# Kernel optimization log

Measured on AMD Instinct MI355X. Metric: run time of the kernel, lower is better.

## Reference

```python
import jax, jax.numpy as jnp
import numpy as np

B = 1024
IN_SIZE = 8192
OUT_SIZE = 8192
CONNECTIVITY = 32
NNZ = OUT_SIZE * CONNECTIVITY  # 262144


def setup_inputs() -> dict:
    key = jax.random.key(0)
    kx, kv, ki = jax.random.split(key, 3)
    x = jax.random.normal(kx, (B, IN_SIZE), dtype=jnp.float32)
    # uniform init as in module: (rand-0.5)*2*sqrt(3/connectivity)
    scale = np.sqrt(3.0 / CONNECTIVITY)
    values = (jax.random.uniform(kv, (NNZ,), dtype=jnp.float32) - 0.5) * 2.0 * scale
    # indices_out = list(range(out_size)) * connectivity -> arange(nnz) % out_size
    idx_out = (jnp.arange(NNZ) % OUT_SIZE).astype(jnp.int32)
    # uniform distribution: randperm(nnz) % in_size ~ uniform over [0, in_size)
    idx_in = jax.random.randint(ki, (NNZ,), 0, IN_SIZE, dtype=jnp.int32)
    return {"x": x, "values": values, "idx_out": idx_out, "idx_in": idx_in,
            "out_size": OUT_SIZE}


def reference(x, values, idx_out, idx_in, out_size):
    # y[b, o] = sum over nnz k with idx_out[k]==o of values[k] * x[b, idx_in[k]]
    # (spmm(indices, values, out, in, x.T).T in the original)
    contrib = x[:, idx_in] * values[None, :]          # [B, nnz]
    y = jnp.zeros((x.shape[0], out_size), dtype=x.dtype)
    y = y.at[:, idx_out].add(contrib)                 # scatter-add over output rows
    return y
```

## Files before the change

kernel.cpp:

```cpp
#include <hip/hip_runtime.h>

#define IN_SIZE   8192
#define OUT_SIZE  8192
#define CONN      32
#define NNZ       (OUT_SIZE * CONN)
#define BATCH     1024
#define BT        4
#define OT        4096
#define NTHREADS  512
#define OPT       (OT / NTHREADS)

typedef int          int4v   __attribute__((ext_vector_type(4)));
typedef float        float4v __attribute__((ext_vector_type(4)));
typedef unsigned int uint2v  __attribute__((ext_vector_type(2)));
typedef unsigned int uint4v  __attribute__((ext_vector_type(4)));

__device__ __forceinline__ unsigned bf16rne(float f) {
  unsigned u = __builtin_bit_cast(unsigned, f);
  return (u + 0x7fffu + ((u >> 16) & 1u)) >> 16;
}

__global__ __launch_bounds__(256)
void pack_kernel(const float* __restrict__ values,
                 const int*   __restrict__ idx_in,
                 unsigned int* __restrict__ pk) {
  int k = blockIdx.x * 256 + threadIdx.x;
  if (k < NNZ) {
    unsigned u = __builtin_bit_cast(unsigned, values[k]);
    unsigned r = (u + 0xFFFu + ((u >> 13) & 1u)) >> 13;
    pk[k] = ((unsigned)idx_in[k] << 19) | (r & 0x7FFFFu);
  }
}

template<bool PACKED>
__global__ __launch_bounds__(NTHREADS, 4)
void spl_kernel(const float* __restrict__ x,
                const unsigned int* __restrict__ pk,
                const float* __restrict__ values,
                const int* __restrict__ idx_in,
                float* __restrict__ y) {
  __shared__ unsigned long long xs[IN_SIZE];

  const int s  = blockIdx.x & 15;
  const int g  = blockIdx.x >> 4;
  const int oh = s >> 3;
  const int bb = g * 8 + (s & 7);
  const int b0 = bb * BT;
  const int o0 = oh * OT + threadIdx.x * OPT;

  {
    const float4v* r0 = (const float4v*)(x + (size_t)(b0 + 0) * IN_SIZE);
    const float4v* r1 = (const float4v*)(x + (size_t)(b0 + 1) * IN_SIZE);
    const float4v* r2 = (const float4v*)(x + (size_t)(b0 + 2) * IN_SIZE);
    const float4v* r3 = (const float4v*)(x + (size_t)(b0 + 3) * IN_SIZE);
    #pragma unroll
    for (int pass = 0; pass < IN_SIZE / (NTHREADS * 4); ++pass) {
      int c4 = pass * NTHREADS + threadIdx.x;
      float4v a = r0[c4], b = r1[c4], c = r2[c4], d = r3[c4];
      #pragma unroll
      for (int q = 0; q < 4; ++q) {
        unsigned lo = bf16rne(a[q]) | (bf16rne(b[q]) << 16);
        unsigned hi = bf16rne(c[q]) | (bf16rne(d[q]) << 16);
        xs[c4 * 4 + q] = ((unsigned long long)hi << 32) | lo;
      }
    }
  }
  __syncthreads();

  float acc[OPT][BT];
  #pragma unroll
  for (int q = 0; q < OPT; ++q)
    #pragma unroll
    for (int bt = 0; bt < BT; ++bt) acc[q][bt] = 0.0f;

  const char* xsb = (const char*)xs;

  #pragma unroll 2
  for (int j = 0; j < CONN; ++j) {
    const int kb = j * OUT_SIZE + o0;
    unsigned pv[OPT];
    if constexpr (PACKED) {
      uint4v p0 = *(const uint4v*)(pk + kb);
      uint4v p1 = *(const uint4v*)(pk + kb + 4);
      pv[0]=p0.x; pv[1]=p0.y; pv[2]=p0.z; pv[3]=p0.w;
      pv[4]=p1.x; pv[5]=p1.y; pv[6]=p1.z; pv[7]=p1.w;
      #pragma unroll
      for (int q = 0; q < OPT; ++q) {
        unsigned p = pv[q];
        float v = __builtin_bit_cast(float, p << 13);
        uint2v gv = *(const uint2v*)(xsb + ((p >> 16) & 0x1FFF8u));
        float x0 = __builtin_bit_cast(float, gv.x << 16);
        float x1 = __builtin_bit_cast(float, gv.x & 0xFFFF0000u);
        float x2 = __builtin_bit_cast(float, gv.y << 16);
        float x3 = __builtin_bit_cast(float, gv.y & 0xFFFF0000u);
        acc[q][0] += v * x0;
        acc[q][1] += v * x1;
        acc[q][2] += v * x2;
        acc[q][3] += v * x3;
      }
    } else {
      int4v  i0 = *(const int4v*)(idx_in + kb);
      int4v  i1 = *(const int4v*)(idx_in + kb + 4);
      float4v v0 = *(const float4v*)(values + kb);
      float4v v1 = *(const float4v*)(values + kb + 4);
      int   iv[OPT] = {i0.x,i0.y,i0.z,i0.w,i1.x,i1.y,i1.z,i1.w};
      float vv[OPT] = {v0.x,v0.y,v0.z,v0.w,v1.x,v1.y,v1.z,v1.w};
      #pragma unroll
      for (int q = 0; q < OPT; ++q) {
        float v = vv[q];
        uint2v gv = *(const uint2v*)(xsb + ((unsigned)iv[q] << 3));
        float x0 = __builtin_bit_cast(float, gv.x << 16);
        float x1 = __builtin_bit_cast(float, gv.x & 0xFFFF0000u);
        float x2 = __builtin_bit_cast(float, gv.y << 16);
        float x3 = __builtin_bit_cast(float, gv.y & 0xFFFF0000u);
        acc[q][0] += v * x0;
        acc[q][1] += v * x1;
        acc[q][2] += v * x2;
        acc[q][3] += v * x3;
      }
    }
  }

  #pragma unroll
  for (int bt = 0; bt < BT; ++bt) {
    float* yr = y + (size_t)(b0 + bt) * OUT_SIZE + o0;
    float4v w0 = {acc[0][bt], acc[1][bt], acc[2][bt], acc[3][bt]};
    float4v w1 = {acc[4][bt], acc[5][bt], acc[6][bt], acc[7][bt]};
    __builtin_nontemporal_store(w0, (float4v*)yr);
    __builtin_nontemporal_store(w1, (float4v*)(yr + 4));
  }
}

extern "C" void kernel_launch(void* const* d_in, const int* in_sizes, int n_in,
                              void* d_out, int out_size, void* d_ws, size_t ws_size,
                              hipStream_t stream) {
  const float* x      = (const float*)d_in[0];
  const float* values = (const float*)d_in[1];
  const int*   idx_in = (const int*)d_in[3];
  float*       y      = (float*)d_out;

  const dim3 grid((BATCH / BT) * (OUT_SIZE / OT));
  const dim3 blk(NTHREADS);

  if (ws_size >= (size_t)NNZ * sizeof(unsigned int)) {
    unsigned int* pk = (unsigned int*)d_ws;
    hipLaunchKernelGGL(pack_kernel, dim3(NNZ / 256), dim3(256), 0, stream,
                       values, idx_in, pk);
    hipLaunchKernelGGL((spl_kernel<true>), grid, blk, 0, stream,
                       x, pk, values, idx_in, y);
  } else {
    hipLaunchKernelGGL((spl_kernel<false>), grid, blk, 0, stream,
                       x, nullptr, values, idx_in, y);
  }
}
```

Baseline: 36.19 us.

## Tile eight batch rows per block with 128-bit LDS gathers and permuted index layout

Doubles the batch tile to eight rows packed as bf16 into 16-byte LDS entries (128 KB shared per block) and doubles the thread count, so each output row handles four outputs instead of eight. Each LDS gather now feeds eight FMAs instead of four, halving gather instructions and the number of passes over the index/value stream. The LDS layout is permuted (index split by low two bits) so the staging writes are contiguous, and the pack kernel pre-permutes indices to match. The trade-off is one block per CU due to LDS size, lower occupancy, and a serialised staging phase without the grid swizzle used before.

```diff
diff --git a/kernel.cpp b/kernel.cpp
--- a/kernel.cpp
+++ b/kernel.cpp
@@ -5,14 +5,13 @@
 #define CONN      32
 #define NNZ       (OUT_SIZE * CONN)
 #define BATCH     1024
-#define BT        4
+#define BT        8
 #define OT        4096
-#define NTHREADS  512
+#define NTHREADS  1024
 #define OPT       (OT / NTHREADS)
 
 typedef int          int4v   __attribute__((ext_vector_type(4)));
 typedef float        float4v __attribute__((ext_vector_type(4)));
-typedef unsigned int uint2v  __attribute__((ext_vector_type(2)));
 typedef unsigned int uint4v  __attribute__((ext_vector_type(4)));
 
 __device__ __forceinline__ unsigned bf16rne(float f) {
@@ -28,41 +27,43 @@
   if (k < NNZ) {
     unsigned u = __builtin_bit_cast(unsigned, values[k]);
     unsigned r = (u + 0xFFFu + ((u >> 13) & 1u)) >> 13;
-    pk[k] = ((unsigned)idx_in[k] << 19) | (r & 0x7FFFFu);
+    unsigned i = (unsigned)idx_in[k];
+    unsigned s = ((i & 3u) << 11) | (i >> 2);
+    pk[k] = (s << 19) | (r & 0x7FFFFu);
   }
 }
 
 template<bool PACKED>
-__global__ __launch_bounds__(NTHREADS, 4)
+__global__ __launch_bounds__(NTHREADS)
 void spl_kernel(const float* __restrict__ x,
                 const unsigned int* __restrict__ pk,
                 const float* __restrict__ values,
                 const int* __restrict__ idx_in,
                 float* __restrict__ y) {
-  __shared__ unsigned long long xs[IN_SIZE];
+  __shared__ uint4v xs[IN_SIZE];
 
-  const int s  = blockIdx.x & 15;
-  const int g  = blockIdx.x >> 4;
-  const int oh = s >> 3;
-  const int bb = g * 8 + (s & 7);
-  const int b0 = bb * BT;
-  const int o0 = oh * OT + threadIdx.x * OPT;
+  const int bid = blockIdx.x;
+  const int oh  = bid >> 7;
+  const int bb  = bid & 127;
+  const int b0  = bb * BT;
+  const int t   = threadIdx.x;
+  const int o0  = oh * OT + t * OPT;
 
-  {
-    const float4v* r0 = (const float4v*)(x + (size_t)(b0 + 0) * IN_SIZE);
-    const float4v* r1 = (const float4v*)(x + (size_t)(b0 + 1) * IN_SIZE);
-    const float4v* r2 = (const float4v*)(x + (size_t)(b0 + 2) * IN_SIZE);
-    const float4v* r3 = (const float4v*)(x + (size_t)(b0 + 3) * IN_SIZE);
+  #pragma unroll
+  for (int p = 0; p < IN_SIZE / (NTHREADS * 4); ++p) {
+    int c4 = p * NTHREADS + t;
+    float4v r[BT];
     #pragma unroll
-    for (int pass = 0; pass < IN_SIZE / (NTHREADS * 4); ++pass) {
-      int c4 = pass * NTHREADS + threadIdx.x;
-      float4v a = r0[c4], b = r1[c4], c = r2[c4], d = r3[c4];
-      #pragma unroll
-      for (int q = 0; q < 4; ++q) {
-        unsigned lo = bf16rne(a[q]) | (bf16rne(b[q]) << 16);
-        unsigned hi = bf16rne(c[q]) | (bf16rne(d[q]) << 16);
-        xs[c4 * 4 + q] = ((unsigned long long)hi << 32) | lo;
-      }
+    for (int b = 0; b < BT; ++b)
+      r[b] = *(const float4v*)(x + (size_t)(b0 + b) * IN_SIZE + c4 * 4);
+    #pragma unroll
+    for (int q = 0; q < 4; ++q) {
+      uint4v w;
+      w.x = bf16rne(r[0][q]) | (bf16rne(r[1][q]) << 16);
+      w.y = bf16rne(r[2][q]) | (bf16rne(r[3][q]) << 16);
+      w.z = bf16rne(r[4][q]) | (bf16rne(r[5][q]) << 16);
+      w.w = bf16rne(r[6][q]) | (bf16rne(r[7][q]) << 16);
+      xs[q * 2048 + c4] = w;
     }
   }
   __syncthreads();
@@ -81,53 +82,39 @@
     unsigned pv[OPT];
     if constexpr (PACKED) {
       uint4v p0 = *(const uint4v*)(pk + kb);
-      uint4v p1 = *(const uint4v*)(pk + kb + 4);
-      pv[0]=p0.x; pv[1]=p0.y; pv[2]=p0.z; pv[3]=p0.w;
-      pv[4]=p1.x; pv[5]=p1.y; pv[6]=p1.z; pv[7]=p1.w;
+      pv[0] = p0.x; pv[1] = p0.y; pv[2] = p0.z; pv[3] = p0.w;
+    } else {
+      int4v i0 = *(const int4v*)(idx_in + kb);
+      float4v v0 = *(const float4v*)(values + kb);
       #pragma unroll
       for (int q = 0; q < OPT; ++q) {
-        unsigned p = pv[q];
-        float v = __builtin_bit_cast(float, p << 13);
-        uint2v gv = *(const uint2v*)(xsb + ((p >> 16) & 0x1FFF8u));
-        float x0 = __builtin_bit_cast(float, gv.x << 16);
-        float x1 = __builtin_bit_cast(float, gv.x & 0xFFFF0000u);
-        float x2 = __builtin_bit_cast(float, gv.y << 16);
-        float x3 = __builtin_bit_cast(float, gv.y & 0xFFFF0000u);
-        acc[q][0] += v * x0;
-        acc[q][1] += v * x1;
-        acc[q][2] += v * x2;
-        acc[q][3] += v * x3;
+        unsigned u = __builtin_bit_cast(unsigned, v0[q]);
+        unsigned r = (u >> 13) & 0x7FFFFu;
+        unsigned i = (unsigned)i0[q];
+        pv[q] = ((((i & 3u) << 11) | (i >> 2)) << 19) | r;
       }
-    } else {
-      int4v  i0 = *(const int4v*)(idx_in + kb);
-      int4v  i1 = *(const int4v*)(idx_in + kb + 4);
-      float4v v0 = *(const float4v*)(values + kb);
-      float4v v1 = *(const float4v*)(values + kb + 4);
-      int   iv[OPT] = {i0.x,i0.y,i0.z,i0.w,i1.x,i1.y,i1.z,i1.w};
-      float vv[OPT] = {v0.x,v0.y,v0.z,v0.w,v1.x,v1.y,v1.z,v1.w};
-      #pragma unroll
-      for (int q = 0; q < OPT; ++q) {
-        float v = vv[q];
-        uint2v gv = *(const uint2v*)(xsb + ((unsigned)iv[q] << 3));
-        float x0 = __builtin_bit_cast(float, gv.x << 16);
-        float x1 = __builtin_bit_cast(float, gv.x & 0xFFFF0000u);
-        float x2 = __builtin_bit_cast(float, gv.y << 16);
-        float x3 = __builtin_bit_cast(float, gv.y & 0xFFFF0000u);
-        acc[q][0] += v * x0;
-        acc[q][1] += v * x1;
-        acc[q][2] += v * x2;
-        acc[q][3] += v * x3;
-      }
+    }
+    #pragma unroll
+    for (int q = 0; q < OPT; ++q) {
+      unsigned p = pv[q];
+      float v = __builtin_bit_cast(float, p << 13);
+      uint4v gv = *(const uint4v*)(xsb + ((p >> 15) & 0x1FFF0u));
+      acc[q][0] += v * __builtin_bit_cast(float, gv.x << 16);
+      acc[q][1] += v * __builtin_bit_cast(float, gv.x & 0xFFFF0000u);
+      acc[q][2] += v * __builtin_bit_cast(float, gv.y << 16);
+      acc[q][3] += v * __builtin_bit_cast(float, gv.y & 0xFFFF0000u);
+      acc[q][4] += v * __builtin_bit_cast(float, gv.z << 16);
+      acc[q][5] += v * __builtin_bit_cast(float, gv.z & 0xFFFF0000u);
+      acc[q][6] += v * __builtin_bit_cast(float, gv.w << 16);
+      acc[q][7] += v * __builtin_bit_cast(float, gv.w & 0xFFFF0000u);
     }
   }
 
   #pragma unroll
   for (int bt = 0; bt < BT; ++bt) {
     float* yr = y + (size_t)(b0 + bt) * OUT_SIZE + o0;
-    float4v w0 = {acc[0][bt], acc[1][bt], acc[2][bt], acc[3][bt]};
-    float4v w1 = {acc[4][bt], acc[5][bt], acc[6][bt], acc[7][bt]};
-    __builtin_nontemporal_store(w0, (float4v*)yr);
-    __builtin_nontemporal_store(w1, (float4v*)(yr + 4));
+    float4v w = {acc[0][bt], acc[1][bt], acc[2][bt], acc[3][bt]};
+    __builtin_nontemporal_store(w, (float4v*)yr);
   }
 }
 
```

Result: faster. 34.82 us (-3.8%).
